# Kernel tuning notes

Measured on AMD Instinct MI355X. Metric: run time of the kernel, lower is better.

The kernel has to match this reference:

```python
import jax, jax.numpy as jnp
import numpy as np

N_NODES = 100000
N_EDGES = 1600000
NUM_FEATURES = 128
HIDDEN = 64
NUM_CLASSES = 16


def setup_inputs() -> dict:
    key = jax.random.key(0)
    k1, k2, k3, k4 = jax.random.split(key, 4)
    x = jax.random.normal(k1, (N_NODES, NUM_FEATURES), dtype=jnp.float32)
    edge_index = jax.random.randint(k2, (2, N_EDGES), 0, N_NODES, dtype=jnp.int64)
    # Glorot-ish scaled weights ([in, out] layout; PyG stores [out,in] but math is x @ W)
    W1 = jax.random.normal(k3, (NUM_FEATURES, HIDDEN), dtype=jnp.float32) * (1.0 / np.sqrt(NUM_FEATURES))
    W2 = jax.random.normal(k4, (HIDDEN, NUM_CLASSES), dtype=jnp.float32) * (1.0 / np.sqrt(HIDDEN))
    return {"x": x, "edge_index": edge_index, "W1": W1, "W2": W2}


def _gcn_conv(x, edge_index, W):
    # GCNConv(add_self_loops=False, bias=False): linear then sym-normalized scatter-add.
    n = x.shape[0]
    row, col = edge_index[0], edge_index[1]  # source -> target
    h = x @ W  # [N, out]
    # degree from unit edge weights scattered on target nodes
    deg = jax.ops.segment_sum(jnp.ones(row.shape[0], dtype=h.dtype), col, num_segments=n)
    deg_inv_sqrt = jnp.where(deg > 0, jax.lax.rsqrt(jnp.maximum(deg, 1.0)), 0.0)
    norm = deg_inv_sqrt[row] * deg_inv_sqrt[col]  # [E]
    msg = h[row] * norm[:, None]  # gather + scale, [E, out]
    return jax.ops.segment_sum(msg, col, num_segments=n)  # scatter-add to targets


def reference(x, edge_index, W1, W2):
    h = _gcn_conv(x, edge_index, W1)
    h = _gcn_conv(h, edge_index, W2)
    return jax.nn.log_softmax(h, axis=1)
```

## Files before the change

kernel.cpp:

```cpp
#include <hip/hip_runtime.h>
#include <hip/hip_bf16.h>
#include <hip/hip_fp16.h>


#define STRIDE 48
#define BCAP   3072


__global__ __launch_bounds__(512) void k_bucket(const int* __restrict__ ei,
                                                const void* __restrict__ xv,
                                                const void* __restrict__ W1v,
                                                const void* __restrict__ W2v,
                                                int* __restrict__ flags,
                                                float* __restrict__ W12,
                                                int* __restrict__ bcnt,
                                                int* __restrict__ buf,
                                                int e, int n, int nb) {
    __shared__ int hist[1024];
    __shared__ int basec[1024];
    __shared__ float wtmp[2048];
    __shared__ int sraw, sbad;
    int t = threadIdx.x;
    int b = blockIdx.x;

    if (t == 0) { sraw = 0; sbad = 0; }
    for (int i = t; i < nb; i += 512) hist[i] = 0;
    __syncthreads();

    {
        int i = b * 4096 + t;
        if (i < e && ei[2 * (size_t)i + 1] != 0) atomicOr(&sraw, 1);
    }
    if (b < 8) {
        const unsigned short* xs = (const unsigned short*)xv;
        int bad = 0;
        for (int i = t; i < 1024; i += 512) {
            unsigned ex2 = (xs[i] >> 7) & 0xFF;
            if (ex2 >= 0x90) bad = 1;
        }
        if (bad) atomicOr(&sbad, 1);
    }
    __syncthreads();
    int raw = sraw ? 0 : 1;

    if (b < 8) {
        bool f32 = sbad != 0;
        if (f32) {
            const float* W1 = (const float*)W1v;
            const float* W2 = (const float*)W2v;
            for (int i = t; i < 1024; i += 512) {
                wtmp[i] = W1[b * 1024 + i];
                wtmp[1024 + i] = W2[i];
            }
        } else {
            const __hip_bfloat16* W1 = (const __hip_bfloat16*)W1v;
            const __hip_bfloat16* W2 = (const __hip_bfloat16*)W2v;
            for (int i = t; i < 1024; i += 512) {
                wtmp[i] = __bfloat162float(W1[b * 1024 + i]);
                wtmp[1024 + i] = __bfloat162float(W2[i]);
            }
        }
    }

    int e0 = b * 4096;
    int bk[8], rec[8];
#pragma unroll
    for (int j = 0; j < 8; ++j) {
        int i = e0 + j * 512 + t;
        bk[j] = -1;
        if (i < e) {
            int r, c;
            if (raw) {
                r = ((const int2*)ei)[(size_t)i].x;
                c = ((const int2*)ei)[(size_t)e + i].x;
            } else {
                r = ei[i];
                c = ei[(size_t)e + i];
            }
            if ((unsigned)c < (unsigned)n && (unsigned)r < (unsigned)n) {
                bk[j] = c >> 7;
                rec[j] = ((c & 127) << 17) | r;
                atomicAdd(&hist[bk[j]], 1);
            }
        }
    }
    __syncthreads();

    if (b < 8 && t < 256) {
        int kl = t >> 4, c = t & 15;
        float acc = 0.0f;
#pragma unroll 8
        for (int f = 0; f < 64; ++f) acc += wtmp[kl * 64 + f] * wtmp[1024 + f * 16 + c];
        W12[(16 * b + kl) * 16 + c] = acc;
        if (b == 0 && t == 0) { flags[0] = sbad; flags[1] = raw; }
    }

    for (int i = t; i < nb; i += 512) {
        int h = hist[i];
        basec[i] = h ? atomicAdd(&bcnt[i], h) : 0;
    }
    __syncthreads();
#pragma unroll
    for (int j = 0; j < 8; ++j) {
        if (bk[j] >= 0) {
            int slot = atomicAdd(&basec[bk[j]], 1);
            if (slot < BCAP) buf[(size_t)bk[j] * BCAP + slot] = rec[j];
        }
    }
}


__global__ __launch_bounds__(256) void k_csr(const int* __restrict__ bcnt,
                                             const int* __restrict__ buf,
                                             int* __restrict__ cnt,
                                             int* __restrict__ csr, int n) {
    __shared__ int lcnt[128];
    __shared__ int lcsr[128 * STRIDE];
    int t = threadIdx.x;
    int b = blockIdx.x;
    if (t < 128) lcnt[t] = 0;
    int4 zero4 = {0, 0, 0, 0};
    for (int i = t; i < 128 * STRIDE / 4; i += 256) ((int4*)lcsr)[i] = zero4;
    __syncthreads();

    int m = bcnt[b];
    if (m > BCAP) m = BCAP;
    for (int i = t; i < m; i += 256) {
        int rec = buf[(size_t)b * BCAP + i];
        int cl = rec >> 17;
        int r = rec & 0x1FFFF;
        int slot = atomicAdd(&lcnt[cl], 1);
        if (slot < STRIDE) lcsr[cl * STRIDE + slot] = r;
    }
    __syncthreads();
    int node = (b << 7) + t;
    if (t < 128 && node < n) cnt[node] = lcnt[t];
    const int4* src = (const int4*)lcsr;
    int4* dst = (int4*)csr + (size_t)b * (128 * STRIDE / 4);
    for (int i = t; i < 128 * STRIDE / 4; i += 256) dst[i] = src[i];
}


__global__ __launch_bounds__(512) void k_z(const void* __restrict__ xv,
                                           const float* __restrict__ W12,
                                           const int* __restrict__ flags,
                                           const int* __restrict__ cnt,
                                           __half* __restrict__ z, int n) {
    __shared__ float ws[2048];
    __shared__ float part[4][128][17];
    int t = threadIdx.x;
    int b = blockIdx.x;
    int node_l = t & 127;
    int kq = t >> 7;
    int node0 = (b << 7) + node_l;
    int node = node0 < n ? node0 : n - 1;

    for (int i = t; i < 2048; i += 512) ws[i] = W12[i];
    __syncthreads();

    float acc[16];
#pragma unroll
    for (int c = 0; c < 16; ++c) acc[c] = 0.0f;

    if (flags[0]) {
        const float4* x4 = (const float4*)xv + (size_t)node * 32 + kq * 8;
#pragma unroll
        for (int j = 0; j < 8; ++j) {
            float4 v = x4[j];
            float xk[4] = {v.x, v.y, v.z, v.w};
#pragma unroll
            for (int q = 0; q < 4; ++q) {
                const float* w = &ws[(kq * 32 + j * 4 + q) * 16];
                float xx = xk[q];
#pragma unroll
                for (int c = 0; c < 16; ++c) acc[c] += xx * w[c];
            }
        }
    } else {
        const uint4* x4 = (const uint4*)xv + (size_t)node * 16 + kq * 4;
#pragma unroll
        for (int j = 0; j < 4; ++j) {
            uint4 v = x4[j];
            float xk[8];
            xk[0] = __uint_as_float(v.x << 16);
            xk[1] = __uint_as_float(v.x & 0xffff0000u);
            xk[2] = __uint_as_float(v.y << 16);
            xk[3] = __uint_as_float(v.y & 0xffff0000u);
            xk[4] = __uint_as_float(v.z << 16);
            xk[5] = __uint_as_float(v.z & 0xffff0000u);
            xk[6] = __uint_as_float(v.w << 16);
            xk[7] = __uint_as_float(v.w & 0xffff0000u);
#pragma unroll
            for (int q = 0; q < 8; ++q) {
                const float* w = &ws[(kq * 32 + j * 8 + q) * 16];
                float xx = xk[q];
#pragma unroll
                for (int c = 0; c < 16; ++c) acc[c] += xx * w[c];
            }
        }
    }

#pragma unroll
    for (int c = 0; c < 16; ++c) part[kq][node_l][c] = acc[c];
    __syncthreads();

    int nl2 = t >> 2;
    int cg = (t & 3) * 4;
    int node2 = (b << 7) + nl2;
    if (node2 < n) {
        float s0 = part[0][nl2][cg + 0] + part[1][nl2][cg + 0] + part[2][nl2][cg + 0] + part[3][nl2][cg + 0];
        float s1 = part[0][nl2][cg + 1] + part[1][nl2][cg + 1] + part[2][nl2][cg + 1] + part[3][nl2][cg + 1];
        float s2 = part[0][nl2][cg + 2] + part[1][nl2][cg + 2] + part[2][nl2][cg + 2] + part[3][nl2][cg + 2];
        float s3 = part[0][nl2][cg + 3] + part[1][nl2][cg + 3] + part[2][nl2][cg + 3] + part[3][nl2][cg + 3];
        int deg = cnt[node2];
        float di = (deg > 0) ? rsqrtf((float)deg) : 0.0f;
        __half2 h0 = __halves2half2(__float2half(s0 * di), __float2half(s1 * di));
        __half2 h1 = __halves2half2(__float2half(s2 * di), __float2half(s3 * di));
        uint2 u;
        u.x = *(unsigned*)&h0;
        u.y = *(unsigned*)&h1;
        ((uint2*)(z + (size_t)node2 * 16))[t & 3] = u;
    }
}


__global__ __launch_bounds__(256) void k_agg1b(const int* __restrict__ cnt,
                                               const int* __restrict__ csr,
                                               const __half* __restrict__ z,
                                               __half* __restrict__ z2, int n) {
    int t = threadIdx.x;
    int wid = t >> 6, lane = t & 63;
    int half = lane >> 5, l5 = lane & 31;
    int node0 = blockIdx.x * 8 + wid * 2 + half;
    int node = node0 < n ? node0 : n - 1;
    int id  = csr[(size_t)node * STRIDE + l5];
    int id2 = csr[(size_t)node * STRIDE + 32 + (l5 & 15)];
    int deg = cnt[node];
    float di = (deg > 0) ? rsqrtf((float)deg) : 0.0f;
    int m = deg < STRIDE ? deg : STRIDE;
    int sub = l5 >> 3, f2 = l5 & 7;
    int base = half << 5;
    const __half2* zp = (const __half2*)z;
    float ax = 0.0f, ay = 0.0f;
#pragma unroll
    for (int j = 0; j < 24; j += 4) {
        int s = __shfl(id, base + j + sub);
        float2 v = __half22float2(zp[(size_t)s * 8 + f2]);
        bool ok = (j + sub) < m;
        ax += ok ? v.x : 0.0f;
        ay += ok ? v.y : 0.0f;
    }
    for (int j = 24; j < m; j += 4) {
        int sidx = j + sub;
        int s = (j < 32) ? __shfl(id, base + sidx)
                         : __shfl(id2, base + (sidx & 15));
        if (sidx < m) {
            float2 v = __half22float2(zp[(size_t)s * 8 + f2]);
            ax += v.x;
            ay += v.y;
        }
    }
    ax += __shfl_xor(ax, 8);  ay += __shfl_xor(ay, 8);
    ax += __shfl_xor(ax, 16); ay += __shfl_xor(ay, 16);
    float s2 = di * di;
    if (node0 < n && l5 < 8)
        ((__half2*)z2)[(size_t)node * 8 + l5] =
            __halves2half2(__float2half(ax * s2), __float2half(ay * s2));
}


__global__ __launch_bounds__(256) void k_agg2b(const int* __restrict__ cnt,
                                               const int* __restrict__ csr,
                                               const __half* __restrict__ z2,
                                               const int* __restrict__ flags,
                                               void* __restrict__ outv, int n) {
    int t = threadIdx.x;
    int wid = t >> 6, lane = t & 63;
    int half = lane >> 5, l5 = lane & 31;
    int node0 = blockIdx.x * 8 + wid * 2 + half;
    int node = node0 < n ? node0 : n - 1;
    int id  = csr[(size_t)node * STRIDE + l5];
    int id2 = csr[(size_t)node * STRIDE + 32 + (l5 & 15)];
    int deg = cnt[node];
    float di = (deg > 0) ? rsqrtf((float)deg) : 0.0f;
    int m = deg < STRIDE ? deg : STRIDE;
    int sub = l5 >> 3, f2 = l5 & 7;
    int base = half << 5;
    const __half2* zp = (const __half2*)z2;
    float ax = 0.0f, ay = 0.0f;
#pragma unroll
    for (int j = 0; j < 24; j += 4) {
        int s = __shfl(id, base + j + sub);
        float2 v = __half22float2(zp[(size_t)s * 8 + f2]);
        bool ok = (j + sub) < m;
        ax += ok ? v.x : 0.0f;
        ay += ok ? v.y : 0.0f;
    }
    for (int j = 24; j < m; j += 4) {
        int sidx = j + sub;
        int s = (j < 32) ? __shfl(id, base + sidx)
                         : __shfl(id2, base + (sidx & 15));
        if (sidx < m) {
            float2 v = __half22float2(zp[(size_t)s * 8 + f2]);
            ax += v.x;
            ay += v.y;
        }
    }
    ax += __shfl_xor(ax, 8);  ay += __shfl_xor(ay, 8);
    ax += __shfl_xor(ax, 16); ay += __shfl_xor(ay, 16);
    float vx = ax * di, vy = ay * di;
    float mx = fmaxf(vx, vy);
#pragma unroll
    for (int d = 1; d <= 4; d <<= 1) mx = fmaxf(mx, __shfl_xor(mx, d));
    float es = __expf(vx - mx) + __expf(vy - mx);
#pragma unroll
    for (int d = 1; d <= 4; d <<= 1) es += __shfl_xor(es, d);
    float ls = __logf(es);
    float rx = vx - mx - ls, ry = vy - mx - ls;
    if (node0 < n && l5 < 8) {
        if (flags[0]) {
            float2 r; r.x = rx; r.y = ry;
            ((float2*)outv)[(size_t)node * 8 + l5] = r;
        } else {
            __hip_bfloat162 hh;
            hh.x = __float2bfloat16(rx);
            hh.y = __float2bfloat16(ry);
            ((__hip_bfloat162*)outv)[(size_t)node * 8 + l5] = hh;
        }
    }
}


extern "C" void kernel_launch(void* const* d_in, const int* in_sizes, int n_in,
                              void* d_out, int out_size, void* d_ws, size_t ws_size,
                              hipStream_t stream) {
    const int F = 128, C = 16;
    int n = in_sizes[0] / F;
    int e = in_sizes[1] / 2;
    int nb = (n + 127) >> 7;

    const void* x = d_in[0];
    const int* ei = (const int*)d_in[1];
    const void* W1 = d_in[2];
    const void* W2 = d_in[3];

    char* p = (char*)d_ws;
    auto carve = [&](size_t bytes) {
        char* r = p;
        p += (bytes + 255) & ~(size_t)255;
        return r;
    };
    int*    flags = (int*)  carve(256);
    int*    bcnt  = (int*)  carve((size_t)nb * 4);
    int*    cnt   = (int*)  carve((size_t)n * 4);
    float*  W12   = (float*)carve(128 * 16 * 4);
    int*    csr   = (int*)  carve(((size_t)nb * 128 * STRIDE + 64) * 4);
    __half* z     = (__half*)carve((size_t)n * C * 2);
    size_t buf_sz = (size_t)nb * BCAP * 4;
    size_t z2_sz = (size_t)n * C * 2;
    char* regionB = carve(buf_sz > z2_sz ? buf_sz : z2_sz);
    int*    buf = (int*)regionB;
    __half* z2  = (__half*)regionB;
    (void)ws_size;

    int gb_bucket = (e + 4095) / 4096;
    if (gb_bucket < 8) gb_bucket = 8;

    hipMemsetAsync(bcnt, 0, (size_t)nb * 4, stream);
    k_bucket<<<gb_bucket, 512, 0, stream>>>(ei, x, W1, W2, flags, W12, bcnt, buf, e, n, nb);
    k_csr<<<nb, 256, 0, stream>>>(bcnt, buf, cnt, csr, n);
    k_z<<<nb, 512, 0, stream>>>(x, W12, flags, cnt, z, n);
    k_agg1b<<<(n + 7) / 8, 256, 0, stream>>>(cnt, csr, z, z2, n);
    k_agg2b<<<(n + 7) / 8, 256, 0, stream>>>(cnt, csr, z2, flags, d_out, n);
}
```

Baseline: 166.5 us.

## Build padded CSR directly with global atomics, dropping bucket pass

Replaces the two-pass bucket-then-local-sort CSR construction with a single kernel that does a global atomicAdd on each target node's count and writes the source index straight into a fixed-stride CSR slot. A memset now zeroes both the count and CSR regions in one span. This removes one kernel launch and the intermediate bucket buffer round-trip. In exchange it uses 1.6M scattered global atomics and scattered 4-byte writes, plus a larger memset of the full padded CSR array.

```diff
diff --git a/kernel.cpp b/kernel.cpp
--- a/kernel.cpp
+++ b/kernel.cpp
@@ -4,37 +4,33 @@
 
 
 #define STRIDE 48
-#define BCAP   3072
-
-
-__global__ __launch_bounds__(512) void k_bucket(const int* __restrict__ ei,
-                                                const void* __restrict__ xv,
-                                                const void* __restrict__ W1v,
-                                                const void* __restrict__ W2v,
-                                                int* __restrict__ flags,
-                                                float* __restrict__ W12,
-                                                int* __restrict__ bcnt,
-                                                int* __restrict__ buf,
-                                                int e, int n, int nb) {
-    __shared__ int hist[1024];
-    __shared__ int basec[1024];
+
+
+__global__ __launch_bounds__(256) void k_build(const int* __restrict__ ei,
+                                               const void* __restrict__ xv,
+                                               const void* __restrict__ W1v,
+                                               const void* __restrict__ W2v,
+                                               int* __restrict__ flags,
+                                               float* __restrict__ W12,
+                                               int* __restrict__ cnt,
+                                               int* __restrict__ csr,
+                                               int e, int n) {
     __shared__ float wtmp[2048];
     __shared__ int sraw, sbad;
     int t = threadIdx.x;
     int b = blockIdx.x;
 
     if (t == 0) { sraw = 0; sbad = 0; }
-    for (int i = t; i < nb; i += 512) hist[i] = 0;
     __syncthreads();
 
     {
-        int i = b * 4096 + t;
+        int i = b * 2048 + t;
         if (i < e && ei[2 * (size_t)i + 1] != 0) atomicOr(&sraw, 1);
     }
     if (b < 8) {
         const unsigned short* xs = (const unsigned short*)xv;
         int bad = 0;
-        for (int i = t; i < 1024; i += 512) {
+        for (int i = t; i < 1024; i += 256) {
             unsigned ex2 = (xs[i] >> 7) & 0xFF;
             if (ex2 >= 0x90) bad = 1;
         }
@@ -48,26 +44,26 @@
         if (f32) {
             const float* W1 = (const float*)W1v;
             const float* W2 = (const float*)W2v;
-            for (int i = t; i < 1024; i += 512) {
+            for (int i = t; i < 1024; i += 256) {
                 wtmp[i] = W1[b * 1024 + i];
                 wtmp[1024 + i] = W2[i];
             }
         } else {
             const __hip_bfloat16* W1 = (const __hip_bfloat16*)W1v;
             const __hip_bfloat16* W2 = (const __hip_bfloat16*)W2v;
-            for (int i = t; i < 1024; i += 512) {
+            for (int i = t; i < 1024; i += 256) {
                 wtmp[i] = __bfloat162float(W1[b * 1024 + i]);
                 wtmp[1024 + i] = __bfloat162float(W2[i]);
             }
         }
     }
 
-    int e0 = b * 4096;
-    int bk[8], rec[8];
+    int e0 = b * 2048;
+    int rr[8], cc[8];
 #pragma unroll
     for (int j = 0; j < 8; ++j) {
-        int i = e0 + j * 512 + t;
-        bk[j] = -1;
+        int i = e0 + j * 256 + t;
+        rr[j] = -1;
         if (i < e) {
             int r, c;
             if (raw) {
@@ -78,15 +74,21 @@
                 c = ei[(size_t)e + i];
             }
             if ((unsigned)c < (unsigned)n && (unsigned)r < (unsigned)n) {
-                bk[j] = c >> 7;
-                rec[j] = ((c & 127) << 17) | r;
-                atomicAdd(&hist[bk[j]], 1);
-            }
-        }
-    }
-    __syncthreads();
-
-    if (b < 8 && t < 256) {
+                rr[j] = r;
+                cc[j] = c;
+            }
+        }
+    }
+#pragma unroll
+    for (int j = 0; j < 8; ++j) {
+        if (rr[j] >= 0) {
+            int slot = atomicAdd(&cnt[cc[j]], 1);
+            if (slot < STRIDE) csr[(size_t)cc[j] * STRIDE + slot] = rr[j];
+        }
+    }
+
+    __syncthreads();
+    if (b < 8) {
         int kl = t >> 4, c = t & 15;
         float acc = 0.0f;
 #pragma unroll 8
@@ -94,50 +96,6 @@
         W12[(16 * b + kl) * 16 + c] = acc;
         if (b == 0 && t == 0) { flags[0] = sbad; flags[1] = raw; }
     }
-
-    for (int i = t; i < nb; i += 512) {
-        int h = hist[i];
-        basec[i] = h ? atomicAdd(&bcnt[i], h) : 0;
-    }
-    __syncthreads();
-#pragma unroll
-    for (int j = 0; j < 8; ++j) {
-        if (bk[j] >= 0) {
-            int slot = atomicAdd(&basec[bk[j]], 1);
-            if (slot < BCAP) buf[(size_t)bk[j] * BCAP + slot] = rec[j];
-        }
-    }
-}
-
-
-__global__ __launch_bounds__(256) void k_csr(const int* __restrict__ bcnt,
-                                             const int* __restrict__ buf,
-                                             int* __restrict__ cnt,
-                                             int* __restrict__ csr, int n) {
-    __shared__ int lcnt[128];
-    __shared__ int lcsr[128 * STRIDE];
-    int t = threadIdx.x;
-    int b = blockIdx.x;
-    if (t < 128) lcnt[t] = 0;
-    int4 zero4 = {0, 0, 0, 0};
-    for (int i = t; i < 128 * STRIDE / 4; i += 256) ((int4*)lcsr)[i] = zero4;
-    __syncthreads();
-
-    int m = bcnt[b];
-    if (m > BCAP) m = BCAP;
-    for (int i = t; i < m; i += 256) {
-        int rec = buf[(size_t)b * BCAP + i];
-        int cl = rec >> 17;
-        int r = rec & 0x1FFFF;
-        int slot = atomicAdd(&lcnt[cl], 1);
-        if (slot < STRIDE) lcsr[cl * STRIDE + slot] = r;
-    }
-    __syncthreads();
-    int node = (b << 7) + t;
-    if (t < 128 && node < n) cnt[node] = lcnt[t];
-    const int4* src = (const int4*)lcsr;
-    int4* dst = (int4*)csr + (size_t)b * (128 * STRIDE / 4);
-    for (int i = t; i < 128 * STRIDE / 4; i += 256) dst[i] = src[i];
 }
 
 
@@ -351,24 +309,21 @@
         return r;
     };
     int*    flags = (int*)  carve(256);
-    int*    bcnt  = (int*)  carve((size_t)nb * 4);
+    float*  W12   = (float*)carve(128 * 16 * 4);
+    size_t  csr_bytes = ((size_t)nb * 128 * STRIDE + 64) * 4;
     int*    cnt   = (int*)  carve((size_t)n * 4);
-    float*  W12   = (float*)carve(128 * 16 * 4);
-    int*    csr   = (int*)  carve(((size_t)nb * 128 * STRIDE + 64) * 4);
+    int*    csr   = (int*)  carve(csr_bytes);
     __half* z     = (__half*)carve((size_t)n * C * 2);
-    size_t buf_sz = (size_t)nb * BCAP * 4;
-    size_t z2_sz = (size_t)n * C * 2;
-    char* regionB = carve(buf_sz > z2_sz ? buf_sz : z2_sz);
-    int*    buf = (int*)regionB;
-    __half* z2  = (__half*)regionB;
+    __half* z2    = (__half*)carve((size_t)n * C * 2);
     (void)ws_size;
 
-    int gb_bucket = (e + 4095) / 4096;
-    if (gb_bucket < 8) gb_bucket = 8;
-
-    hipMemsetAsync(bcnt, 0, (size_t)nb * 4, stream);
-    k_bucket<<<gb_bucket, 512, 0, stream>>>(ei, x, W1, W2, flags, W12, bcnt, buf, e, n, nb);
-    k_csr<<<nb, 256, 0, stream>>>(bcnt, buf, cnt, csr, n);
+    size_t zspan = (size_t)((char*)csr - (char*)cnt) + csr_bytes;
+    hipMemsetAsync(cnt, 0, zspan, stream);
+
+    int gb = (e + 2047) / 2048;
+    if (gb < 8) gb = 8;
+
+    k_build<<<gb, 256, 0, stream>>>(ei, x, W1, W2, flags, W12, cnt, csr, e, n);
     k_z<<<nb, 512, 0, stream>>>(x, W12, flags, cnt, z, n);
     k_agg1b<<<(n + 7) / 8, 256, 0, stream>>>(cnt, csr, z, z2, n);
     k_agg2b<<<(n + 7) / 8, 256, 0, stream>>>(cnt, csr, z2, flags, d_out, n);
```

After: 277.5 us. 1.67x slower.

## Sort edges locally by bucket before scattering and widen buckets to 256 nodes

Applied to the files above, without the earlier changes.

The bucketing kernel now counting-sorts its 4096 edges in shared memory by destination bucket (prefix scan plus staging), then writes them out contiguously so each bucket's records land in coalesced runs instead of scattered single-int stores. Buckets widen from 128 to 256 nodes, which halves the bucket count, and the CSR kernel moves to 512 threads and a larger LDS tile. The cost is a 512-step Hillis-Steele scan with many barriers, more shared memory per block, and a per-node CSR layout that still relies on the fixed 48-slot stride. The hist arrays are now fixed at 512 entries, so node counts above 131072 would overflow them.

```diff
diff --git a/kernel.cpp b/kernel.cpp
--- a/kernel.cpp
+++ b/kernel.cpp
@@ -4,7 +4,7 @@
 
 
 #define STRIDE 48
-#define BCAP   3072
+#define BCAP   6144
 
 
 __global__ __launch_bounds__(512) void k_bucket(const int* __restrict__ ei,
@@ -16,15 +16,19 @@
                                                 int* __restrict__ bcnt,
                                                 int* __restrict__ buf,
                                                 int e, int n, int nb) {
-    __shared__ int hist[1024];
-    __shared__ int basec[1024];
+    __shared__ int hist[512];
+    __shared__ int scn[512];
+    __shared__ int cur[512];
+    __shared__ int gb[512];
     __shared__ float wtmp[2048];
-    __shared__ int sraw, sbad;
+    __shared__ int srt[4096];
+    __shared__ unsigned short key[4096];
+    __shared__ int sraw, sbad, tot;
     int t = threadIdx.x;
     int b = blockIdx.x;
 
     if (t == 0) { sraw = 0; sbad = 0; }
-    for (int i = t; i < nb; i += 512) hist[i] = 0;
+    hist[t] = 0;
     __syncthreads();
 
     {
@@ -78,13 +82,48 @@
                 c = ei[(size_t)e + i];
             }
             if ((unsigned)c < (unsigned)n && (unsigned)r < (unsigned)n) {
-                bk[j] = c >> 7;
-                rec[j] = ((c & 127) << 17) | r;
+                bk[j] = c >> 8;
+                rec[j] = ((c & 255) << 17) | r;
                 atomicAdd(&hist[bk[j]], 1);
             }
         }
     }
     __syncthreads();
+
+    scn[t] = hist[t];
+    __syncthreads();
+#pragma unroll
+    for (int off = 1; off < 512; off <<= 1) {
+        int add = (t >= off) ? scn[t - off] : 0;
+        __syncthreads();
+        scn[t] += add;
+        __syncthreads();
+    }
+    {
+        int h = hist[t];
+        cur[t] = scn[t] - h;
+        gb[t] = h ? atomicAdd(&bcnt[t], h) : 0;
+        if (t == 511) tot = scn[511];
+    }
+    __syncthreads();
+
+#pragma unroll
+    for (int j = 0; j < 8; ++j) {
+        if (bk[j] >= 0) {
+            int s = atomicAdd(&cur[bk[j]], 1);
+            srt[s] = rec[j];
+            key[s] = (unsigned short)bk[j];
+        }
+    }
+    __syncthreads();
+
+    int total = tot;
+    for (int i = t; i < total; i += 512) {
+        int k = key[i];
+        int excl = cur[k] - hist[k];
+        int slot = gb[k] + (i - excl);
+        if (slot < BCAP) buf[(size_t)k * BCAP + slot] = srt[i];
+    }
 
     if (b < 8 && t < 256) {
         int kl = t >> 4, c = t & 15;
@@ -94,38 +133,25 @@
         W12[(16 * b + kl) * 16 + c] = acc;
         if (b == 0 && t == 0) { flags[0] = sbad; flags[1] = raw; }
     }
-
-    for (int i = t; i < nb; i += 512) {
-        int h = hist[i];
-        basec[i] = h ? atomicAdd(&bcnt[i], h) : 0;
-    }
-    __syncthreads();
-#pragma unroll
-    for (int j = 0; j < 8; ++j) {
-        if (bk[j] >= 0) {
-            int slot = atomicAdd(&basec[bk[j]], 1);
-            if (slot < BCAP) buf[(size_t)bk[j] * BCAP + slot] = rec[j];
-        }
-    }
-}
-
-
-__global__ __launch_bounds__(256) void k_csr(const int* __restrict__ bcnt,
+}
+
+
+__global__ __launch_bounds__(512) void k_csr(const int* __restrict__ bcnt,
                                              const int* __restrict__ buf,
                                              int* __restrict__ cnt,
                                              int* __restrict__ csr, int n) {
-    __shared__ int lcnt[128];
-    __shared__ int lcsr[128 * STRIDE];
+    __shared__ int lcnt[256];
+    __shared__ int lcsr[256 * STRIDE];
     int t = threadIdx.x;
     int b = blockIdx.x;
-    if (t < 128) lcnt[t] = 0;
+    if (t < 256) lcnt[t] = 0;
     int4 zero4 = {0, 0, 0, 0};
-    for (int i = t; i < 128 * STRIDE / 4; i += 256) ((int4*)lcsr)[i] = zero4;
+    for (int i = t; i < 256 * STRIDE / 4; i += 512) ((int4*)lcsr)[i] = zero4;
     __syncthreads();
 
     int m = bcnt[b];
     if (m > BCAP) m = BCAP;
-    for (int i = t; i < m; i += 256) {
+    for (int i = t; i < m; i += 512) {
         int rec = buf[(size_t)b * BCAP + i];
         int cl = rec >> 17;
         int r = rec & 0x1FFFF;
@@ -133,11 +159,11 @@
         if (slot < STRIDE) lcsr[cl * STRIDE + slot] = r;
     }
     __syncthreads();
-    int node = (b << 7) + t;
-    if (t < 128 && node < n) cnt[node] = lcnt[t];
+    int node = (b << 8) + t;
+    if (t < 256 && node < n) cnt[node] = lcnt[t];
     const int4* src = (const int4*)lcsr;
-    int4* dst = (int4*)csr + (size_t)b * (128 * STRIDE / 4);
-    for (int i = t; i < 128 * STRIDE / 4; i += 256) dst[i] = src[i];
+    int4* dst = (int4*)csr + (size_t)b * (256 * STRIDE / 4);
+    for (int i = t; i < 256 * STRIDE / 4; i += 512) dst[i] = src[i];
 }
 
 
@@ -337,7 +363,8 @@
     const int F = 128, C = 16;
     int n = in_sizes[0] / F;
     int e = in_sizes[1] / 2;
-    int nb = (n + 127) >> 7;
+    int nb = (n + 255) >> 8;
+    int nz = (n + 127) >> 7;
 
     const void* x = d_in[0];
     const int* ei = (const int*)d_in[1];
@@ -354,7 +381,7 @@
     int*    bcnt  = (int*)  carve((size_t)nb * 4);
     int*    cnt   = (int*)  carve((size_t)n * 4);
     float*  W12   = (float*)carve(128 * 16 * 4);
-    int*    csr   = (int*)  carve(((size_t)nb * 128 * STRIDE + 64) * 4);
+    int*    csr   = (int*)  carve(((size_t)nb * 256 * STRIDE + 64) * 4);
     __half* z     = (__half*)carve((size_t)n * C * 2);
     size_t buf_sz = (size_t)nb * BCAP * 4;
     size_t z2_sz = (size_t)n * C * 2;
@@ -368,8 +395,8 @@
 
     hipMemsetAsync(bcnt, 0, (size_t)nb * 4, stream);
     k_bucket<<<gb_bucket, 512, 0, stream>>>(ei, x, W1, W2, flags, W12, bcnt, buf, e, n, nb);
-    k_csr<<<nb, 256, 0, stream>>>(bcnt, buf, cnt, csr, n);
-    k_z<<<nb, 512, 0, stream>>>(x, W12, flags, cnt, z, n);
+    k_csr<<<nb, 512, 0, stream>>>(bcnt, buf, cnt, csr, n);
+    k_z<<<nz, 512, 0, stream>>>(x, W12, flags, cnt, z, n);
     k_agg1b<<<(n + 7) / 8, 256, 0, stream>>>(cnt, csr, z, z2, n);
     k_agg2b<<<(n + 7) / 8, 256, 0, stream>>>(cnt, csr, z2, flags, d_out, n);
 }
```

New measurement: 162.8 us. -2.2%, faster.
